# Performance work log

Measured on AMD Instinct MI355X. Metric: run time of the kernel, lower is better.

## Reference

```python
import jax, jax.numpy as jnp
import numpy as np

D = 256; NH = 8; NL = 3; NP = 4; DFF = 1024; NENC = 3; NDEC = 3; BS = 8
SHAPES = ((60, 60), (30, 30), (15, 15))
NQ = 3600

def _linear(x, W, b):
    return x @ W.T + b

def _ln(x, g, b, eps=1e-5):
    m = x.mean(-1, keepdims=True)
    v = ((x - m) ** 2).mean(-1, keepdims=True)
    return (x - m) / jnp.sqrt(v + eps) * g + b

def _pos_embed(h, w):
    # PositionEmbeddingSine(num_pos_feats=D//2, normalize=True)
    npf = D // 2
    scale = 2.0 * np.pi; eps = 1e-6
    ye = jnp.arange(1, h + 1, dtype=jnp.float32) / (h + eps) * scale
    xe = jnp.arange(1, w + 1, dtype=jnp.float32) / (w + eps) * scale
    dim_t = 10000.0 ** (2.0 * (jnp.arange(npf) // 2).astype(jnp.float32) / npf)
    def inter(p):  # interleave sin/cos like torch stack(...,4).flatten(3)
        return jnp.stack([jnp.sin(p[:, 0::2]), jnp.cos(p[:, 1::2])], -1).reshape(p.shape[0], npf)
    px = inter(xe[:, None] / dim_t)  # [w, npf]
    py = inter(ye[:, None] / dim_t)  # [h, npf]
    pos = jnp.concatenate([jnp.broadcast_to(py[:, None, :], (h, w, npf)),
                           jnp.broadcast_to(px[None, :, :], (h, w, npf))], -1)
    return pos.reshape(h * w, D)

def _grid(H, W):
    ry = (jnp.arange(H, dtype=jnp.float32) + 0.5) / H
    rx = (jnp.arange(W, dtype=jnp.float32) + 0.5) / W
    gy, gx = jnp.meshgrid(ry, rx, indexing='ij')
    return jnp.stack([gx.reshape(-1), gy.reshape(-1)], -1)

def _ref_enc():
    ref = jnp.concatenate([_grid(H, W) for (H, W) in SHAPES], 0)
    return jnp.broadcast_to(ref[None, :, None, :], (1, ref.shape[0], NL, 2))

def _ref_dec():
    ref = _grid(60, 60)  # hardcoded in DecoderLayer.get_reference_points
    return jnp.broadcast_to(ref[None, :, None, :], (1, NQ, NL, 2))

def _bilinear(v, x, y, H, W):
    # v: [N,h,HW,dh], x/y: [N,Lq,h,P] in pixel coords (grid_sample align_corners=False, zero padding)
    N, h, _, dh = v.shape
    Lq, P = x.shape[1], x.shape[3]
    x0 = jnp.floor(x); y0 = jnp.floor(y)
    wx1 = x - x0; wy1 = y - y0
    acc = jnp.zeros((N, h, Lq * P, dh), v.dtype)
    for dx, dy in ((0, 0), (1, 0), (0, 1), (1, 1)):
        xi = x0 + dx; yi = y0 + dy
        wgt = (wx1 if dx else 1.0 - wx1) * (wy1 if dy else 1.0 - wy1)
        valid = (xi >= 0) & (xi < W) & (yi >= 0) & (yi < H)
        idx = (jnp.clip(yi, 0, H - 1) * W + jnp.clip(xi, 0, W - 1)).astype(jnp.int32)
        idx = idx.transpose(0, 2, 1, 3).reshape(N, h, Lq * P)
        g = jnp.take_along_axis(v, idx[..., None], axis=2)
        wv = jnp.where(valid, wgt, 0.0).transpose(0, 2, 1, 3).reshape(N, h, Lq * P)
        acc = acc + g * wv[..., None]
    return acc.reshape(N, h, Lq, P, dh).transpose(0, 2, 1, 3, 4)  # [N,Lq,h,P,dh]

def _msda(query, ref, src, offW, offb, awW, awb, vpW, vpb, opW, opb):
    # Deformable-DETR MSDeformAttn
    N, Lq, d = query.shape
    h = NH; dh = d // h; P = NP
    value = _linear(src, vpW, vpb).reshape(N, -1, h, dh)
    off = _linear(query, offW, offb).reshape(N, Lq, h, NL, P, 2)
    aw = jax.nn.softmax(_linear(query, awW, awb).reshape(N, Lq, h, NL * P), -1).reshape(N, Lq, h, NL, P)
    norm = jnp.array([[W_, H_] for (H_, W_) in SHAPES], dtype=jnp.float32)
    loc = ref[:, :, None, :, None, :] + off / norm[None, None, None, :, None, :]
    out = jnp.zeros((N, Lq, h, dh), query.dtype)
    start = 0
    for l, (H_, W_) in enumerate(SHAPES):
        v = value[:, start:start + H_ * W_].transpose(0, 2, 1, 3)  # [N,h,HW,dh]
        start += H_ * W_
        lx = loc[:, :, :, l, :, 0] * W_ - 0.5
        ly = loc[:, :, :, l, :, 1] * H_ - 0.5
        s = _bilinear(v, lx, ly, H_, W_)
        out = out + (s * aw[:, :, :, l, :, None]).sum(3)
    return _linear(out.reshape(N, Lq, d), opW, opb)

def _mha(q, k, v, Wi, bi, Wo, bo):
    # torch nn.MultiheadAttention, inputs (L, N, E)
    L, N, E = q.shape
    h = NH; hd = E // h
    qp = _linear(q, Wi[:E], bi[:E]).reshape(L, N, h, hd)
    kp = _linear(k, Wi[E:2 * E], bi[E:2 * E]).reshape(L, N, h, hd)
    vp = _linear(v, Wi[2 * E:], bi[2 * E:]).reshape(L, N, h, hd)
    sc = jnp.einsum('lnhd,snhd->nhls', qp, kp) / np.float32(np.sqrt(hd))
    a = jax.nn.softmax(sc, -1)
    o = jnp.einsum('nhls,snhd->lnhd', a, vp).reshape(L, N, E)
    return _linear(o, Wo, bo)

def _forward(feat0, feat1, feat2, context, query_embed, level_embed, enc_off_W, enc_off_b, enc_aw_W, enc_aw_b, enc_vp_W, enc_vp_b, enc_op_W, enc_op_b, enc_fc1_W, enc_fc1_b, enc_fc2_W, enc_fc2_b, enc_ln1_g, enc_ln1_b, enc_ln2_g, enc_ln2_b, dec_off_W, dec_off_b, dec_aw_W, dec_aw_b, dec_vp_W, dec_vp_b, dec_op_W, dec_op_b, dec_fc1_W, dec_fc1_b, dec_fc2_W, dec_fc2_b, dec_ln1_g, dec_ln1_b, dec_ln2_g, dec_ln2_b, dec_sa_in_W, dec_sa_in_b, dec_sa_out_W, dec_sa_out_b, dec_ln3_g, dec_ln3_b):
    srcs, poss = [], []
    for l, (f, (H, W)) in enumerate(zip((feat0, feat1, feat2), SHAPES)):
        srcs.append(f.reshape(BS, D, H * W).transpose(0, 2, 1))
        pe = _pos_embed(H, W) + level_embed[l]
        poss.append(jnp.broadcast_to(pe[None], (BS, H * W, D)))
    src = jnp.concatenate(srcs, 1)   # [BS, S, D]
    pos = jnp.concatenate(poss, 1)
    ref_e = _ref_enc()
    out = src
    for i in range(NENC):
        a = _msda(out + pos, ref_e, out, enc_off_W[i], enc_off_b[i], enc_aw_W[i], enc_aw_b[i], enc_vp_W[i], enc_vp_b[i], enc_op_W[i], enc_op_b[i])
        out = _ln(out + a, enc_ln1_g[i], enc_ln1_b[i])
        f2 = _linear(jax.nn.relu(_linear(out, enc_fc1_W[i], enc_fc1_b[i])), enc_fc2_W[i], enc_fc2_b[i])
        out = _ln(out + f2, enc_ln2_g[i], enc_ln2_b[i])
    memory = out
    tgt = context + query_embed[:, None, :]  # [NQ, BS, D]
    ref_d = _ref_dec()
    for i in range(NDEC):
        # faithful to original: q.transpose(0,1) feeds MHA with (L=BS, N=NQ)
        q = tgt.transpose(1, 0, 2)
        t2 = _mha(q, q, q, dec_sa_in_W[i], dec_sa_in_b[i], dec_sa_out_W[i], dec_sa_out_b[i]).transpose(1, 0, 2)
        tgt = _ln(tgt + t2, dec_ln2_g[i], dec_ln2_b[i])
        tq = tgt.transpose(1, 0, 2)  # [BS, NQ, D]
        t2 = _msda(tq, ref_d, memory, dec_off_W[i], dec_off_b[i], dec_aw_W[i], dec_aw_b[i], dec_vp_W[i], dec_vp_b[i], dec_op_W[i], dec_op_b[i])
        tq = _ln(tq + t2, dec_ln1_g[i], dec_ln1_b[i])
        f2 = _linear(jax.nn.relu(_linear(tq, dec_fc1_W[i], dec_fc1_b[i])), dec_fc2_W[i], dec_fc2_b[i])
        tq = _ln(tq + f2, dec_ln3_g[i], dec_ln3_b[i])
        tgt = tq.transpose(1, 0, 2)
    return tgt  # [NQ, BS, D]

def setup_inputs() -> dict:
    key = jax.random.key(0)
    ks = iter(jax.random.split(key, 64))
    def rn(shape, s=1.0):
        return jax.random.normal(next(ks), shape, jnp.float32) * s
    inp = {}
    inp['feat0'] = rn((BS, D, 60, 60))
    inp['feat1'] = rn((BS, D, 30, 30))
    inp['feat2'] = rn((BS, D, 15, 15))
    inp['context'] = rn((NQ, BS, D))
    inp['query_embed'] = rn((NQ, D))
    inp['level_embed'] = rn((NL, D), 0.02)
    HLP2 = NH * NL * NP * 2; HLP = NH * NL * NP
    for pre, n in (('enc', NENC), ('dec', NDEC)):
        inp[pre + '_off_W'] = rn((n, HLP2, D), 0.02)
        inp[pre + '_off_b'] = rn((n, HLP2), 0.02)
        inp[pre + '_aw_W'] = rn((n, HLP, D), 0.02)
        inp[pre + '_aw_b'] = jnp.zeros((n, HLP), jnp.float32)
        inp[pre + '_vp_W'] = rn((n, D, D), 0.02)
        inp[pre + '_vp_b'] = jnp.zeros((n, D), jnp.float32)
        inp[pre + '_op_W'] = rn((n, D, D), 0.02)
        inp[pre + '_op_b'] = jnp.zeros((n, D), jnp.float32)
        inp[pre + '_fc1_W'] = rn((n, DFF, D), 0.02)
        inp[pre + '_fc1_b'] = jnp.zeros((n, DFF), jnp.float32)
        inp[pre + '_fc2_W'] = rn((n, D, DFF), 0.02)
        inp[pre + '_fc2_b'] = jnp.zeros((n, D), jnp.float32)
        inp[pre + '_ln1_g'] = jnp.ones((n, D), jnp.float32)
        inp[pre + '_ln1_b'] = jnp.zeros((n, D), jnp.float32)
        inp[pre + '_ln2_g'] = jnp.ones((n, D), jnp.float32)
        inp[pre + '_ln2_b'] = jnp.zeros((n, D), jnp.float32)
    inp['dec_sa_in_W'] = rn((NDEC, 3 * D, D), 0.02)
    inp['dec_sa_in_b'] = jnp.zeros((NDEC, 3 * D), jnp.float32)
    inp['dec_sa_out_W'] = rn((NDEC, D, D), 0.02)
    inp['dec_sa_out_b'] = jnp.zeros((NDEC, D), jnp.float32)
    inp['dec_ln3_g'] = jnp.ones((NDEC, D), jnp.float32)
    inp['dec_ln3_b'] = jnp.zeros((NDEC, D), jnp.float32)
    return inp

def reference(feat0, feat1, feat2, context, query_embed, level_embed, enc_off_W, enc_off_b, enc_aw_W, enc_aw_b, enc_vp_W, enc_vp_b, enc_op_W, enc_op_b, enc_fc1_W, enc_fc1_b, enc_fc2_W, enc_fc2_b, enc_ln1_g, enc_ln1_b, enc_ln2_g, enc_ln2_b, dec_off_W, dec_off_b, dec_aw_W, dec_aw_b, dec_vp_W, dec_vp_b, dec_op_W, dec_op_b, dec_fc1_W, dec_fc1_b, dec_fc2_W, dec_fc2_b, dec_ln1_g, dec_ln1_b, dec_ln2_g, dec_ln2_b, dec_sa_in_W, dec_sa_in_b, dec_sa_out_W, dec_sa_out_b, dec_ln3_g, dec_ln3_b):
    return _forward(feat0, feat1, feat2, context, query_embed, level_embed, enc_off_W, enc_off_b, enc_aw_W, enc_aw_b, enc_vp_W, enc_vp_b, enc_op_W, enc_op_b, enc_fc1_W, enc_fc1_b, enc_fc2_W, enc_fc2_b, enc_ln1_g, enc_ln1_b, enc_ln2_g, enc_ln2_b, dec_off_W, dec_off_b, dec_aw_W, dec_aw_b, dec_vp_W, dec_vp_b, dec_op_W, dec_op_b, dec_fc1_W, dec_fc1_b, dec_fc2_W, dec_fc2_b, dec_ln1_g, dec_ln1_b, dec_ln2_g, dec_ln2_b, dec_sa_in_W, dec_sa_in_b, dec_sa_out_W, dec_sa_out_b, dec_ln3_g, dec_ln3_b)
```

## Files before the change

kernel.cpp:

```cpp
#include <hip/hip_runtime.h>
#include <cmath>

#define D_MODEL 256
#define NHEADS 8
#define BSZ 8
#define S_TOT 4725
#define NQRY 3600

typedef unsigned short ushortT;
using bf16x8  = __attribute__((ext_vector_type(8))) __bf16;
using floatx4 = __attribute__((ext_vector_type(4))) float;

__device__ __forceinline__ ushortT f2bf(float f)
{
    union { float f; unsigned u; } v; v.f = f;
    unsigned r = v.u + 0x7FFFu + ((v.u >> 16) & 1u);
    return (ushortT)(r >> 16);
}
__device__ __forceinline__ float bf2f(ushortT u)
{
    union { unsigned u; float f; } v; v.u = ((unsigned)u) << 16;
    return v.f;
}
__device__ __forceinline__ float bits2f(unsigned u)
{
    union { unsigned u; float f; } v; v.u = u;
    return v.f;
}

#define GLD16(gp, lp) __builtin_amdgcn_global_load_lds( \
    (const __attribute__((address_space(1))) void*)(gp), \
    (__attribute__((address_space(3))) void*)(lp), 16, 0, 0)

template<int RELU, int OUTBF>
__global__ __launch_bounds__(256) void gemm_bf16_kernel(
    const ushortT* __restrict__ A, const ushortT* __restrict__ W,
    const float* __restrict__ bias, void* __restrict__ Cout,
    int M, int N, int K)
{
    __shared__ ushortT SM[128 * 32 * 2];
    ushortT* As = SM;
    ushortT* Bs = SM + 128 * 32;
    const int tid  = threadIdx.x;
    const int lane = tid & 63;
    const int wid  = tid >> 6;
    const int bm = blockIdx.x * 128;
    const int bn = blockIdx.y * 128;
    const int wm = (wid & 1) * 64;
    const int wn = (wid >> 1) * 64;
    const int col16 = lane & 15;
    const int quad  = lane >> 4;
    const int srow = lane >> 2;
    const int cperm = (lane & 3) ^ ((lane >> 3) & 3);
    const int rxor = (col16 >> 1) & 3;

    floatx4 acc[4][4];
#pragma unroll
    for (int i = 0; i < 4; i++)
#pragma unroll
        for (int j = 0; j < 4; j++) acc[i][j] = (floatx4){0.f, 0.f, 0.f, 0.f};

    const int rbase = wid * 32;
    for (int k0 = 0; k0 < K; k0 += 32) {
        if (k0) __syncthreads();
#pragma unroll
        for (int j = 0; j < 2; j++) {
            int row = rbase + j * 16 + srow;
            int gm = bm + row; if (gm >= M) gm = M - 1;
            GLD16(A + (size_t)gm * K + k0 + cperm * 8, &As[(rbase + j * 16) * 32]);
            int gn = bn + row; if (gn >= N) gn = N - 1;
            GLD16(W + (size_t)gn * K + k0 + cperm * 8, &Bs[(rbase + j * 16) * 32]);
        }
        __syncthreads();
        bf16x8 av[4], bv[4];
#pragma unroll
        for (int i = 0; i < 4; i++) {
            av[i] = *(const bf16x8*)&As[(wm + i * 16 + col16) * 32 + (quad ^ rxor) * 8];
            bv[i] = *(const bf16x8*)&Bs[(wn + i * 16 + col16) * 32 + (quad ^ rxor) * 8];
        }
#pragma unroll
        for (int mi = 0; mi < 4; mi++)
#pragma unroll
            for (int ni = 0; ni < 4; ni++)
                acc[mi][ni] = __builtin_amdgcn_mfma_f32_16x16x32_bf16(
                    av[mi], bv[ni], acc[mi][ni], 0, 0, 0);
    }

    if (OUTBF) {
        __syncthreads();
        ushortT* cs = SM + wid * (16 * 72);
        const int row_l = lane >> 2;
        const int colg  = (lane & 3) * 16;
#pragma unroll
        for (int mi = 0; mi < 4; mi++) {
#pragma unroll
            for (int ni = 0; ni < 4; ni++) {
                int gn = bn + wn + ni * 16 + col16;
                float bs = bias[gn < N ? gn : N - 1];
#pragma unroll
                for (int r = 0; r < 4; r++) {
                    float v = acc[mi][ni][r] + bs;
                    if (RELU) v = fmaxf(v, 0.f);
                    cs[(quad * 4 + r) * 72 + ni * 16 + col16] = f2bf(v);
                }
            }
            int gm = bm + wm + mi * 16 + row_l;
            int gn0 = bn + wn + colg;
            if (gm < M) {
                ushortT* dst = (ushortT*)Cout + (size_t)gm * N + gn0;
                if (gn0 + 8 <= N)  *(uint4*)dst       = *(uint4*)&cs[row_l * 72 + colg];
                if (gn0 + 16 <= N) *(uint4*)(dst + 8) = *(uint4*)&cs[row_l * 72 + colg + 8];
            }
        }
    } else {
#pragma unroll
        for (int ni = 0; ni < 4; ni++) {
            int gn = bn + wn + ni * 16 + col16;
            if (gn >= N) continue;
            float bs = bias[gn];
#pragma unroll
            for (int mi = 0; mi < 4; mi++) {
#pragma unroll
                for (int r = 0; r < 4; r++) {
                    int gm = bm + wm + mi * 16 + quad * 4 + r;
                    if (gm >= M) continue;
                    float v = acc[mi][ni][r] + bs;
                    if (RELU) v = fmaxf(v, 0.f);
                    ((float*)Cout)[(size_t)gm * N + gn] = v;
                }
            }
        }
    }
}

static inline void gemm_bf16(const ushortT* A, const ushortT* W, const float* bias,
                             void* C, int M, int N, int K, int relu, int outbf,
                             hipStream_t s)
{
    dim3 g((M + 127) / 128, (N + 127) / 128);
    if (relu) {
        if (outbf) hipLaunchKernelGGL((gemm_bf16_kernel<1,1>), g, dim3(256), 0, s, A, W, bias, C, M, N, K);
        else       hipLaunchKernelGGL((gemm_bf16_kernel<1,0>), g, dim3(256), 0, s, A, W, bias, C, M, N, K);
    } else {
        if (outbf) hipLaunchKernelGGL((gemm_bf16_kernel<0,1>), g, dim3(256), 0, s, A, W, bias, C, M, N, K);
        else       hipLaunchKernelGGL((gemm_bf16_kernel<0,0>), g, dim3(256), 0, s, A, W, bias, C, M, N, K);
    }
}

__global__ void f2bf_kernel(const float* __restrict__ src, ushortT* __restrict__ dst, int n)
{
    int t = blockIdx.x * blockDim.x + threadIdx.x;
    if (t < n) dst[t] = f2bf(src[t]);
}

__global__ void conv_offaw_kernel(const float* __restrict__ offW, const float* __restrict__ awW,
                                  ushortT* __restrict__ dst)
{
    int t = blockIdx.x * blockDim.x + threadIdx.x;
    if (t >= 3 * 288 * 256) return;
    int c = t & 255;
    int r = (t >> 8) % 288;
    int i = t / (288 * 256);
    float v = (r < 192) ? offW[((size_t)i * 192 + r) * 256 + c]
                        : awW[((size_t)i * 96 + (r - 192)) * 256 + c];
    dst[t] = f2bf(v);
}

__global__ void conv_offaw_bias_kernel(const float* __restrict__ offb, const float* __restrict__ awb,
                                       float* __restrict__ dst)
{
    int t = blockIdx.x * blockDim.x + threadIdx.x;
    if (t >= 3 * 288) return;
    int r = t % 288;
    int i = t / 288;
    dst[t] = (r < 192) ? offb[i * 192 + r] : awb[i * 96 + (r - 192)];
}

__device__ __forceinline__ void level_of(int s, int& l, int& H, int& W, int& hw)
{
    if (s < 3600)      { l = 0; H = 60; W = 60; hw = s; }
    else if (s < 4500) { l = 1; H = 30; W = 30; hw = s - 3600; }
    else               { l = 2; H = 15; W = 15; hw = s - 4500; }
}

__global__ __launch_bounds__(256) void transpose_feat_kernel(
    const float* __restrict__ f, ushortT* __restrict__ Xh, int HW, int s0)
{
    __shared__ float tile[32][33];
    const int b  = blockIdx.z;
    const int hw0 = blockIdx.x * 32;
    const int d0  = blockIdx.y * 32;
    const int tx = threadIdx.x & 31;
    const int ty = threadIdx.x >> 5;
    const float* fb = f + ((size_t)b * 256 + d0) * HW + hw0;
#pragma unroll
    for (int r = ty; r < 32; r += 8) {
        if (hw0 + tx < HW) tile[r][tx] = fb[(size_t)r * HW + tx];
    }
    __syncthreads();
    ushortT* xb = Xh + ((size_t)b * S_TOT + s0 + hw0) * 256 + d0;
#pragma unroll
    for (int r = ty; r < 32; r += 8) {
        if (hw0 + r < HW) xb[(size_t)r * 256 + tx] = f2bf(tile[tx][r]);
    }
}

__global__ void build_pos_kernel(const float* __restrict__ level_embed, float* __restrict__ pos)
{
    int t = blockIdx.x * blockDim.x + threadIdx.x;
    if (t >= S_TOT * D_MODEL) return;
    int d = t & 255;
    int s = t >> 8;
    int l, H, W, hw; level_of(s, l, H, W, hw);
    int y = hw / W, x = hw % W;
    int dd = (d < 128) ? d : d - 128;
    float v = (d < 128)
        ? ((float)(y + 1)) / ((float)H + 1e-6f) * 6.28318530717958647692f
        : ((float)(x + 1)) / ((float)W + 1e-6f) * 6.28318530717958647692f;
    float tpow = powf(10000.f, (float)(2 * (dd >> 1)) * (1.f / 128.f));
    float arg = v / tpow;
    float val = (dd & 1) ? cosf(arg) : sinf(arg);
    pos[t] = val + level_embed[l * D_MODEL + d];
}

__global__ void build_ref_kernel(float* __restrict__ refE, float* __restrict__ refD)
{
    int t = blockIdx.x * blockDim.x + threadIdx.x;
    if (t < S_TOT) {
        int l, H, W, hw; level_of(t, l, H, W, hw);
        int y = hw / W, x = hw % W;
        refE[2 * t]     = ((float)x + 0.5f) / (float)W;
        refE[2 * t + 1] = ((float)y + 0.5f) / (float)H;
    } else if (t < S_TOT + NQRY) {
        int q = t - S_TOT;
        int y = q / 60, x = q % 60;
        refD[2 * q]     = ((float)x + 0.5f) / 60.f;
        refD[2 * q + 1] = ((float)y + 0.5f) / 60.f;
    }
}

__global__ void build_tgt_kernel(const float* __restrict__ context, const float* __restrict__ qe,
                                 ushortT* __restrict__ TGTh)
{
    int t = blockIdx.x * blockDim.x + threadIdx.x;
    if (t >= NQRY * BSZ * 64) return;
    int gi = t & 63;
    int row = t >> 6;
    int nq = row >> 3;
    int d0 = gi * 4;
    const float4 c4 = *(const float4*)(context + (size_t)row * 256 + d0);
    const float4 q4 = *(const float4*)(qe + (size_t)nq * 256 + d0);
    ushortT pk[4] = { f2bf(c4.x + q4.x), f2bf(c4.y + q4.y), f2bf(c4.z + q4.z), f2bf(c4.w + q4.w) };
    *(uint2*)(TGTh + (size_t)row * 256 + d0) = *(uint2*)pk;
}

__global__ void add_pos_kernel(const ushortT* __restrict__ Xh, const float* __restrict__ pos,
                               ushortT* __restrict__ Qh)
{
    int t = blockIdx.x * blockDim.x + threadIdx.x;
    if (t >= BSZ * S_TOT * 64) return;
    int gi = t & 63;
    int row = t >> 6;
    int s = row % S_TOT;
    int d0 = gi * 4;
    ushortT x4[4];
    *(uint2*)x4 = *(const uint2*)(Xh + (size_t)row * 256 + d0);
    const float4 p4 = *(const float4*)(pos + (size_t)s * 256 + d0);
    ushortT pk[4] = { f2bf(bf2f(x4[0]) + p4.x), f2bf(bf2f(x4[1]) + p4.y),
                      f2bf(bf2f(x4[2]) + p4.z), f2bf(bf2f(x4[3]) + p4.w) };
    *(uint2*)(Qh + (size_t)row * 256 + d0) = *(uint2*)pk;
}

#define MROWS 8
__global__ __launch_bounds__(256) void msda_kernel(
    const ushortT* __restrict__ value, const float* __restrict__ oa,
    const float* __restrict__ ref, ushortT* __restrict__ out,
    int mode, int total_rows)
{
    __shared__ float sOff[MROWS][192];
    __shared__ float sW[MROWS][96];
    const int br0 = blockIdx.x * MROWS;

    for (int idx = threadIdx.x; idx < MROWS * 288; idx += 256) {
        int r = idx / 288, c = idx - r * 288;
        int lm = br0 + r;
        float v = (lm < total_rows) ? oa[(size_t)lm * 288 + c] : 0.f;
        if (c < 192) sOff[r][c] = v;
        else         sW[r][c - 192] = v;
    }
    __syncthreads();
    if (threadIdx.x < 64) {
        int r = threadIdx.x >> 3, h = threadIdx.x & 7;
        float* p = &sW[r][h * 12];
        float mx = p[0];
#pragma unroll
        for (int i = 1; i < 12; i++) mx = fmaxf(mx, p[i]);
        float ssum = 0.f;
        float e[12];
#pragma unroll
        for (int i = 0; i < 12; i++) { e[i] = expf(p[i] - mx); ssum += e[i]; }
        float inv = 1.f / ssum;
#pragma unroll
        for (int i = 0; i < 12; i++) p[i] = e[i] * inv;
    }
    __syncthreads();

    const int r  = threadIdx.x >> 5;
    const int h  = (threadIdx.x >> 2) & 7;
    const int cg = threadIdx.x & 3;
    const int lm = br0 + r;
    if (lm >= total_rows) return;
    int b, q;
    if (mode == 0) { b = lm / S_TOT; q = lm - b * S_TOT; }
    else           { q = lm >> 3;    b = lm & 7; }
    const float rx = ref[2 * q], ry = ref[2 * q + 1];
    const float* offp = &sOff[r][h * 24];
    const float* wp   = &sW[r][h * 12];

    float acc[8] = {};
    const int HWs[3][3] = {{60, 60, 0}, {30, 30, 3600}, {15, 15, 4500}};
#pragma unroll
    for (int l = 0; l < 3; l++) {
        const int H = HWs[l][0], W = HWs[l][1], s0 = HWs[l][2];
        const ushortT* vbase = value + ((size_t)b * S_TOT + s0) * 256 + h * 32 + cg * 8;
        const float fW = (float)W, fH = (float)H;
#pragma unroll 1
        for (int p = 0; p < 4; p++) {
            float ox = offp[(l * 4 + p) * 2];
            float oy = offp[(l * 4 + p) * 2 + 1];
            float w  = wp[l * 4 + p];
            float lx = rx * fW + ox - 0.5f;
            float ly = ry * fH + oy - 0.5f;
            float x0f = floorf(lx), y0f = floorf(ly);
            int x0 = (int)x0f, y0 = (int)y0f;
            float wx1 = lx - x0f, wy1 = ly - y0f;
            float mx0 = ((unsigned)x0       < (unsigned)W) ? (1.f - wx1) : 0.f;
            float mx1 = ((unsigned)(x0 + 1) < (unsigned)W) ? wx1         : 0.f;
            float my0 = ((unsigned)y0       < (unsigned)H) ? (1.f - wy1) : 0.f;
            float my1 = ((unsigned)(y0 + 1) < (unsigned)H) ? wy1         : 0.f;
            int xc0 = min(max(x0, 0), W - 1);
            int xc1 = min(max(x0 + 1, 0), W - 1);
            int yc0 = min(max(y0, 0), H - 1);
            int yc1 = min(max(y0 + 1, 0), H - 1);
            const uint4 v00 = *(const uint4*)(vbase + (size_t)(yc0 * W + xc0) * 256);
            const uint4 v01 = *(const uint4*)(vbase + (size_t)(yc0 * W + xc1) * 256);
            const uint4 v10 = *(const uint4*)(vbase + (size_t)(yc1 * W + xc0) * 256);
            const uint4 v11 = *(const uint4*)(vbase + (size_t)(yc1 * W + xc1) * 256);
            float w00 = w * my0 * mx0, w01 = w * my0 * mx1;
            float w10 = w * my1 * mx0, w11 = w * my1 * mx1;
#define ACC4(i, lo00, lo01, lo10, lo11) \
            acc[i] = fmaf(w00, bits2f(lo00), acc[i]); \
            acc[i] = fmaf(w01, bits2f(lo01), acc[i]); \
            acc[i] = fmaf(w10, bits2f(lo10), acc[i]); \
            acc[i] = fmaf(w11, bits2f(lo11), acc[i]);
            ACC4(0, v00.x << 16, v01.x << 16, v10.x << 16, v11.x << 16)
            ACC4(1, v00.x & 0xFFFF0000u, v01.x & 0xFFFF0000u, v10.x & 0xFFFF0000u, v11.x & 0xFFFF0000u)
            ACC4(2, v00.y << 16, v01.y << 16, v10.y << 16, v11.y << 16)
            ACC4(3, v00.y & 0xFFFF0000u, v01.y & 0xFFFF0000u, v10.y & 0xFFFF0000u, v11.y & 0xFFFF0000u)
            ACC4(4, v00.z << 16, v01.z << 16, v10.z << 16, v11.z << 16)
            ACC4(5, v00.z & 0xFFFF0000u, v01.z & 0xFFFF0000u, v10.z & 0xFFFF0000u, v11.z & 0xFFFF0000u)
            ACC4(6, v00.w << 16, v01.w << 16, v10.w << 16, v11.w << 16)
            ACC4(7, v00.w & 0xFFFF0000u, v01.w & 0xFFFF0000u, v10.w & 0xFFFF0000u, v11.w & 0xFFFF0000u)
#undef ACC4
        }
    }
    ushortT pk[8];
#pragma unroll
    for (int i = 0; i < 8; i++) pk[i] = f2bf(acc[i]);
    *(uint4*)(out + (size_t)lm * 256 + h * 32 + cg * 8) = *(uint4*)pk;
}

__global__ void ln_res_kernel(const ushortT* __restrict__ x, const ushortT* __restrict__ a,
                              const float* __restrict__ g, const float* __restrict__ b,
                              ushortT* __restrict__ outh, float* __restrict__ outf, int M)
{
    int wave = threadIdx.x >> 6;
    int lane = threadIdx.x & 63;
    int row = blockIdx.x * 4 + wave;
    if (row >= M) return;
    const int d0 = lane * 4;
    ushortT x4[4], a4[4];
    *(uint2*)x4 = *(const uint2*)(x + (size_t)row * 256 + d0);
    *(uint2*)a4 = *(const uint2*)(a + (size_t)row * 256 + d0);
    float v[4];
    float s = 0.f;
#pragma unroll
    for (int i = 0; i < 4; i++) { v[i] = bf2f(x4[i]) + bf2f(a4[i]); s += v[i]; }
#pragma unroll
    for (int o = 32; o > 0; o >>= 1) s += __shfl_down(s, o);
    s = __shfl(s, 0);
    float mean = s * (1.f / 256.f);
    float vs = 0.f;
#pragma unroll
    for (int i = 0; i < 4; i++) { float d = v[i] - mean; vs += d * d; }
#pragma unroll
    for (int o = 32; o > 0; o >>= 1) vs += __shfl_down(vs, o);
    vs = __shfl(vs, 0);
    float inv = rsqrtf(vs * (1.f / 256.f) + 1e-5f);
    const float4 g4 = *(const float4*)(g + d0);
    const float4 b4 = *(const float4*)(b + d0);
    float o0 = (v[0] - mean) * inv * g4.x + b4.x;
    float o1 = (v[1] - mean) * inv * g4.y + b4.y;
    float o2 = (v[2] - mean) * inv * g4.z + b4.z;
    float o3 = (v[3] - mean) * inv * g4.w + b4.w;
    ushortT pk[4] = { f2bf(o0), f2bf(o1), f2bf(o2), f2bf(o3) };
    *(uint2*)(outh + (size_t)row * 256 + d0) = *(uint2*)pk;
    if (outf) {
        float4 of = { o0, o1, o2, o3 };
        *(float4*)(outf + (size_t)row * 256 + d0) = of;
    }
}

__global__ void mha_kernel(const ushortT* __restrict__ qkv, ushortT* __restrict__ o, int nCnt)
{
    int t = blockIdx.x * blockDim.x + threadIdx.x;
    if (t >= nCnt * 64) return;
    int l = t & 7;
    int h = (t >> 3) & 7;
    int n = t >> 6;
    const ushortT* qp = qkv + (size_t)(n * 8 + l) * 768 + h * 32;
    float q[32];
#pragma unroll
    for (int d = 0; d < 32; d++) q[d] = bf2f(qp[d]);
    float sc[8];
#pragma unroll
    for (int s = 0; s < 8; s++) {
        const ushortT* kp = qkv + (size_t)(n * 8 + s) * 768 + 256 + h * 32;
        float acc = 0.f;
#pragma unroll
        for (int d = 0; d < 32; d++) acc = fmaf(q[d], bf2f(kp[d]), acc);
        sc[s] = acc * 0.17677669529663688f;
    }
    float mx = sc[0];
#pragma unroll
    for (int s = 1; s < 8; s++) mx = fmaxf(mx, sc[s]);
    float sum = 0.f;
#pragma unroll
    for (int s = 0; s < 8; s++) { sc[s] = expf(sc[s] - mx); sum += sc[s]; }
    float inv = 1.f / sum;
    float outv[32] = {};
#pragma unroll
    for (int s = 0; s < 8; s++) {
        const ushortT* vp = qkv + (size_t)(n * 8 + s) * 768 + 512 + h * 32;
        float a = sc[s] * inv;
#pragma unroll
        for (int d = 0; d < 32; d++) outv[d] = fmaf(a, bf2f(vp[d]), outv[d]);
    }
    ushortT* op = o + (size_t)(n * 8 + l) * 256 + h * 32;
#pragma unroll
    for (int d = 0; d < 32; d++) op[d] = f2bf(outv[d]);
}

extern "C" void kernel_launch(void* const* d_in, const int* in_sizes, int n_in,
                              void* d_out, int out_size, void* d_ws, size_t ws_size,
                              hipStream_t stream)
{
    const float* feat0       = (const float*)d_in[0];
    const float* feat1       = (const float*)d_in[1];
    const float* feat2       = (const float*)d_in[2];
    const float* context     = (const float*)d_in[3];
    const float* query_embed = (const float*)d_in[4];
    const float* level_embed = (const float*)d_in[5];
    const float* enc_off_W = (const float*)d_in[6];
    const float* enc_off_b = (const float*)d_in[7];
    const float* enc_aw_W  = (const float*)d_in[8];
    const float* enc_aw_b  = (const float*)d_in[9];
    const float* enc_vp_W  = (const float*)d_in[10];
    const float* enc_vp_b  = (const float*)d_in[11];
    const float* enc_op_W  = (const float*)d_in[12];
    const float* enc_op_b  = (const float*)d_in[13];
    const float* enc_fc1_W = (const float*)d_in[14];
    const float* enc_fc1_b = (const float*)d_in[15];
    const float* enc_fc2_W = (const float*)d_in[16];
    const float* enc_fc2_b = (const float*)d_in[17];
    const float* enc_ln1_g = (const float*)d_in[18];
    const float* enc_ln1_b = (const float*)d_in[19];
    const float* enc_ln2_g = (const float*)d_in[20];
    const float* enc_ln2_b = (const float*)d_in[21];
    const float* dec_off_W = (const float*)d_in[22];
    const float* dec_off_b = (const float*)d_in[23];
    const float* dec_aw_W  = (const float*)d_in[24];
    const float* dec_aw_b  = (const float*)d_in[25];
    const float* dec_vp_W  = (const float*)d_in[26];
    const float* dec_vp_b  = (const float*)d_in[27];
    const float* dec_op_W  = (const float*)d_in[28];
    const float* dec_op_b  = (const float*)d_in[29];
    const float* dec_fc1_W = (const float*)d_in[30];
    const float* dec_fc1_b = (const float*)d_in[31];
    const float* dec_fc2_W = (const float*)d_in[32];
    const float* dec_fc2_b = (const float*)d_in[33];
    const float* dec_ln1_g = (const float*)d_in[34];
    const float* dec_ln1_b = (const float*)d_in[35];
    const float* dec_ln2_g = (const float*)d_in[36];
    const float* dec_ln2_b = (const float*)d_in[37];
    const float* sa_in_W   = (const float*)d_in[38];
    const float* sa_in_b   = (const float*)d_in[39];
    const float* sa_out_W  = (const float*)d_in[40];
    const float* sa_out_b  = (const float*)d_in[41];
    const float* dec_ln3_g = (const float*)d_in[42];
    const float* dec_ln3_b = (const float*)d_in[43];

    const int ME = BSZ * S_TOT;
    const int MD = BSZ * NQRY;
    const int EW = ME * D_MODEL;
    const int DW = MD * D_MODEL;

    char* base = (char*)d_ws;
    size_t off = 0;
    auto alloc = [&](size_t bytes) -> char* {
        char* p = base + off;
        off += (bytes + 255) & ~(size_t)255;
        return p;
    };
    ushortT* Xh    = (ushortT*)alloc((size_t)EW * 2);
    ushortT* Vh    = (ushortT*)alloc((size_t)EW * 2);
    ushortT* TGTh  = (ushortT*)alloc((size_t)DW * 2);
    float*   POSb  = (float*)alloc((size_t)S_TOT * 256 * 4);
    float*   REFEb = (float*)alloc((size_t)S_TOT * 2 * 4);
    float*   REFDb = (float*)alloc((size_t)NQRY * 2 * 4);
    ushortT* Wbf   = (ushortT*)alloc((size_t)5160960 * 2);
    float*   OBIAS = (float*)alloc((size_t)2 * 3 * 288 * 4);
    ushortT* Yh    = (ushortT*)alloc((size_t)ME * 256 * 2);
    char*    R     = alloc((size_t)82252800);
    if (ws_size < off) return;

    ushortT* Qh   = (ushortT*)R;
    float*   OAf  = (float*)(R + 19353600);
    ushortT* OUTh = (ushortT*)(R + 62899200);
    ushortT* HIDh = (ushortT*)R;
    ushortT* QKVh = (ushortT*)R;
    ushortT* SOh  = (ushortT*)(R + 44236800);

    size_t wo = 0;
    auto walloc = [&](size_t elems) -> ushortT* { ushortT* p = Wbf + wo; wo += elems; return p; };
    ushortT* h_enc_offaw = walloc(3 * 288 * 256);
    ushortT* h_enc_vp    = walloc(3 * 65536);
    ushortT* h_enc_op    = walloc(3 * 65536);
    ushortT* h_enc_fc1   = walloc(3 * 262144);
    ushortT* h_enc_fc2   = walloc(3 * 262144);
    ushortT* h_dec_offaw = walloc(3 * 288 * 256);
    ushortT* h_dec_vp    = walloc(3 * 65536);
    ushortT* h_dec_op    = walloc(3 * 65536);
    ushortT* h_dec_fc1   = walloc(3 * 262144);
    ushortT* h_dec_fc2   = walloc(3 * 262144);
    ushortT* h_sa_in     = walloc(3 * 196608);
    ushortT* h_sa_out    = walloc(3 * 65536);
    float* enc_oab = OBIAS;
    float* dec_oab = OBIAS + 3 * 288;

    auto conv = [&](const float* s, ushortT* d, int n) {
        hipLaunchKernelGGL(f2bf_kernel, dim3((n + 255) / 256), dim3(256), 0, stream, s, d, n);
    };
    hipLaunchKernelGGL(conv_offaw_kernel, dim3((3 * 288 * 256 + 255) / 256), dim3(256), 0, stream,
                       enc_off_W, enc_aw_W, h_enc_offaw);
    hipLaunchKernelGGL(conv_offaw_kernel, dim3((3 * 288 * 256 + 255) / 256), dim3(256), 0, stream,
                       dec_off_W, dec_aw_W, h_dec_offaw);
    hipLaunchKernelGGL(conv_offaw_bias_kernel, dim3(4), dim3(256), 0, stream,
                       enc_off_b, enc_aw_b, enc_oab);
    hipLaunchKernelGGL(conv_offaw_bias_kernel, dim3(4), dim3(256), 0, stream,
                       dec_off_b, dec_aw_b, dec_oab);
    conv(enc_vp_W,  h_enc_vp,  3 * 65536);
    conv(enc_op_W,  h_enc_op,  3 * 65536);
    conv(enc_fc1_W, h_enc_fc1, 3 * 262144);
    conv(enc_fc2_W, h_enc_fc2, 3 * 262144);
    conv(dec_vp_W,  h_dec_vp,  3 * 65536);
    conv(dec_op_W,  h_dec_op,  3 * 65536);
    conv(dec_fc1_W, h_dec_fc1, 3 * 262144);
    conv(dec_fc2_W, h_dec_fc2, 3 * 262144);
    conv(sa_in_W,   h_sa_in,   3 * 196608);
    conv(sa_out_W,  h_sa_out,  3 * 65536);

    hipLaunchKernelGGL(build_pos_kernel, dim3((S_TOT * 256 + 255) / 256), dim3(256), 0, stream,
                       level_embed, POSb);
    hipLaunchKernelGGL(build_ref_kernel, dim3((S_TOT + NQRY + 255) / 256), dim3(256), 0, stream,
                       REFEb, REFDb);
    hipLaunchKernelGGL(transpose_feat_kernel, dim3(113, 8, 8), dim3(256), 0, stream,
                       feat0, Xh, 3600, 0);
    hipLaunchKernelGGL(transpose_feat_kernel, dim3(29, 8, 8), dim3(256), 0, stream,
                       feat1, Xh, 900, 3600);
    hipLaunchKernelGGL(transpose_feat_kernel, dim3(8, 8, 8), dim3(256), 0, stream,
                       feat2, Xh, 225, 4500);
    hipLaunchKernelGGL(build_tgt_kernel, dim3((MD * 64 + 255) / 256), dim3(256), 0, stream,
                       context, query_embed, TGTh);

    for (int i = 0; i < 3; i++) {
        gemm_bf16(Xh, h_enc_vp + (size_t)i * 65536, enc_vp_b + i * 256, Vh, ME, 256, 256, 0, 1, stream);
        hipLaunchKernelGGL(add_pos_kernel, dim3((ME * 64 + 255) / 256), dim3(256), 0, stream,
                           Xh, POSb, Qh);
        gemm_bf16(Qh, h_enc_offaw + (size_t)i * 73728, enc_oab + i * 288, OAf, ME, 288, 256, 0, 0, stream);
        hipLaunchKernelGGL(msda_kernel, dim3((ME + MROWS - 1) / MROWS), dim3(256), 0, stream,
                           Vh, OAf, REFEb, OUTh, 0, ME);
        gemm_bf16(OUTh, h_enc_op + (size_t)i * 65536, enc_op_b + i * 256, Yh, ME, 256, 256, 0, 1, stream);
        hipLaunchKernelGGL(ln_res_kernel, dim3((ME + 3) / 4), dim3(256), 0, stream,
                           Xh, Yh, enc_ln1_g + i * 256, enc_ln1_b + i * 256, Xh, (float*)nullptr, ME);
        gemm_bf16(Xh, h_enc_fc1 + (size_t)i * 262144, enc_fc1_b + i * 1024, HIDh, ME, 1024, 256, 1, 1, stream);
        gemm_bf16(HIDh, h_enc_fc2 + (size_t)i * 262144, enc_fc2_b + i * 256, Yh, ME, 256, 1024, 0, 1, stream);
        hipLaunchKernelGGL(ln_res_kernel, dim3((ME + 3) / 4), dim3(256), 0, stream,
                           Xh, Yh, enc_ln2_g + i * 256, enc_ln2_b + i * 256, Xh, (float*)nullptr, ME);
    }

    for (int i = 0; i < 3; i++) {
        gemm_bf16(TGTh, h_sa_in + (size_t)i * 196608, sa_in_b + i * 768, QKVh, MD, 768, 256, 0, 1, stream);
        hipLaunchKernelGGL(mha_kernel, dim3((MD * 8 + 255) / 256), dim3(256), 0, stream,
                           QKVh, SOh, MD / 8);
        gemm_bf16(SOh, h_sa_out + (size_t)i * 65536, sa_out_b + i * 256, Yh, MD, 256, 256, 0, 1, stream);
        hipLaunchKernelGGL(ln_res_kernel, dim3((MD + 3) / 4), dim3(256), 0, stream,
                           TGTh, Yh, dec_ln2_g + i * 256, dec_ln2_b + i * 256, TGTh, (float*)nullptr, MD);
        gemm_bf16(Xh, h_dec_vp + (size_t)i * 65536, dec_vp_b + i * 256, Vh, ME, 256, 256, 0, 1, stream);
        gemm_bf16(TGTh, h_dec_offaw + (size_t)i * 73728, dec_oab + i * 288, OAf, MD, 288, 256, 0, 0, stream);
        hipLaunchKernelGGL(msda_kernel, dim3((MD + MROWS - 1) / MROWS), dim3(256), 0, stream,
                           Vh, OAf, REFDb, OUTh, 1, MD);
        gemm_bf16(OUTh, h_dec_op + (size_t)i * 65536, dec_op_b + i * 256, Yh, MD, 256, 256, 0, 1, stream);
        hipLaunchKernelGGL(ln_res_kernel, dim3((MD + 3) / 4), dim3(256), 0, stream,
                           TGTh, Yh, dec_ln1_g + i * 256, dec_ln1_b + i * 256, TGTh, (float*)nullptr, MD);
        gemm_bf16(TGTh, h_dec_fc1 + (size_t)i * 262144, dec_fc1_b + i * 1024, HIDh, MD, 1024, 256, 1, 1, stream);
        gemm_bf16(HIDh, h_dec_fc2 + (size_t)i * 262144, dec_fc2_b + i * 256, Yh, MD, 256, 1024, 0, 1, stream);
        float* outf = (i == 2) ? (float*)d_out : nullptr;
        hipLaunchKernelGGL(ln_res_kernel, dim3((MD + 3) / 4), dim3(256), 0, stream,
                           TGTh, Yh, dec_ln3_g + i * 256, dec_ln3_b + i * 256, TGTh, outf, MD);
    }
}
```

Baseline: 1.646 ms.

## Fuse residual add and LayerNorm into output-projection and FC2 GEMM epilogues

Adds a GEMM kernel whose tile covers 64 rows by the full 256 output columns. Its epilogue adds the bias and the residual, computes row mean and variance across the four waves through shared memory, and applies LayerNorm. It writes bf16 output in place, plus fp32 output on the final decoder layer. This replaces every GEMM followed by ln_res pair, removing the intermediate Yh buffer round trip and twelve kernel launches. In exchange the GEMM uses narrower 64-row tiles with no double buffering, and the variance is computed as E[x^2]-mean^2, which is slightly less numerically robust.

```diff
diff --git a/kernel.cpp b/kernel.cpp
--- a/kernel.cpp
+++ b/kernel.cpp
@@ -145,6 +145,160 @@
         if (outbf) hipLaunchKernelGGL((gemm_bf16_kernel<0,1>), g, dim3(256), 0, s, A, W, bias, C, M, N, K);
         else       hipLaunchKernelGGL((gemm_bf16_kernel<0,0>), g, dim3(256), 0, s, A, W, bias, C, M, N, K);
     }
+}
+
+template<int HAS_OUTF>
+__global__ __launch_bounds__(256) void gemm_ln_kernel(
+    const ushortT* __restrict__ A, const ushortT* __restrict__ W,
+    const float* __restrict__ bias, const ushortT* __restrict__ X,
+    const float* __restrict__ gg, const float* __restrict__ bb,
+    ushortT* __restrict__ outh, float* __restrict__ outf,
+    int M, int K)
+{
+    __shared__ ushortT SM[320 * 32];
+    __shared__ float rs[64][4];
+    __shared__ float rq[64][4];
+    __shared__ float meanv[64];
+    __shared__ float invv[64];
+    const int tid  = threadIdx.x;
+    const int lane = tid & 63;
+    const int wid  = tid >> 6;
+    const int bm = blockIdx.x * 64;
+    const int wn = wid * 64;
+    const int col16 = lane & 15;
+    const int quad  = lane >> 4;
+    const int srow = lane >> 2;
+    const int cperm = (lane & 3) ^ ((lane >> 3) & 3);
+    const int rxor = (col16 >> 1) & 3;
+
+    floatx4 acc[4][4];
+#pragma unroll
+    for (int i = 0; i < 4; i++)
+#pragma unroll
+        for (int j = 0; j < 4; j++) acc[i][j] = (floatx4){0.f, 0.f, 0.f, 0.f};
+
+    for (int k0 = 0; k0 < K; k0 += 32) {
+        if (k0) __syncthreads();
+#pragma unroll
+        for (int j = 0; j < 5; j++) {
+            int frbase = wid * 80 + j * 16;
+            int fr = frbase + srow;
+            const ushortT* gp;
+            if (fr < 64) {
+                int gm = bm + fr; if (gm >= M) gm = M - 1;
+                gp = A + (size_t)gm * K + k0 + cperm * 8;
+            } else {
+                gp = W + (size_t)(fr - 64) * K + k0 + cperm * 8;
+            }
+            GLD16(gp, &SM[frbase * 32]);
+        }
+        __syncthreads();
+        bf16x8 av[4], bv[4];
+#pragma unroll
+        for (int i = 0; i < 4; i++) {
+            av[i] = *(const bf16x8*)&SM[(i * 16 + col16) * 32 + (quad ^ rxor) * 8];
+            bv[i] = *(const bf16x8*)&SM[(64 + wn + i * 16 + col16) * 32 + (quad ^ rxor) * 8];
+        }
+#pragma unroll
+        for (int mi = 0; mi < 4; mi++)
+#pragma unroll
+            for (int ni = 0; ni < 4; ni++)
+                acc[mi][ni] = __builtin_amdgcn_mfma_f32_16x16x32_bf16(
+                    av[mi], bv[ni], acc[mi][ni], 0, 0, 0);
+    }
+
+    int   gncol[4];
+    float bias4[4], gv[4], bbv[4];
+#pragma unroll
+    for (int ni = 0; ni < 4; ni++) {
+        gncol[ni] = wn + ni * 16 + col16;
+        bias4[ni] = bias[gncol[ni]];
+        gv[ni]    = gg[gncol[ni]];
+        bbv[ni]   = bb[gncol[ni]];
+    }
+
+    float psum[4][4], psq[4][4];
+#pragma unroll
+    for (int mi = 0; mi < 4; mi++) {
+#pragma unroll
+        for (int r = 0; r < 4; r++) {
+            int rowl = mi * 16 + quad * 4 + r;
+            int gmc = bm + rowl; if (gmc >= M) gmc = M - 1;
+            const ushortT* xp = X + (size_t)gmc * 256;
+            float ps = 0.f, pq = 0.f;
+#pragma unroll
+            for (int ni = 0; ni < 4; ni++) {
+                float v = acc[mi][ni][r] + bias4[ni] + bf2f(xp[gncol[ni]]);
+                acc[mi][ni][r] = v;
+                ps += v; pq += v * v;
+            }
+            psum[mi][r] = ps; psq[mi][r] = pq;
+        }
+    }
+#pragma unroll
+    for (int mi = 0; mi < 4; mi++) {
+#pragma unroll
+        for (int r = 0; r < 4; r++) {
+            float ps = psum[mi][r], pq = psq[mi][r];
+#pragma unroll
+            for (int m = 1; m < 16; m <<= 1) {
+                ps += __shfl_xor(ps, m);
+                pq += __shfl_xor(pq, m);
+            }
+            if (col16 == 0) {
+                int rowl = mi * 16 + quad * 4 + r;
+                rs[rowl][wid] = ps;
+                rq[rowl][wid] = pq;
+            }
+        }
+    }
+    __syncthreads();
+    if (tid < 64) {
+        float s = rs[tid][0] + rs[tid][1] + rs[tid][2] + rs[tid][3];
+        float q = rq[tid][0] + rq[tid][1] + rq[tid][2] + rq[tid][3];
+        float mean = s * (1.f / 256.f);
+        float var = q * (1.f / 256.f) - mean * mean;
+        meanv[tid] = mean;
+        invv[tid] = rsqrtf(var + 1e-5f);
+    }
+    __syncthreads();
+
+    ushortT* cs = SM + wid * (16 * 72);
+    const int row_l = lane >> 2;
+    const int colg  = (lane & 3) * 16;
+#pragma unroll
+    for (int mi = 0; mi < 4; mi++) {
+#pragma unroll
+        for (int ni = 0; ni < 4; ni++) {
+#pragma unroll
+            for (int r = 0; r < 4; r++) {
+                int rowl = mi * 16 + quad * 4 + r;
+                float outv = (acc[mi][ni][r] - meanv[rowl]) * invv[rowl] * gv[ni] + bbv[ni];
+                cs[(quad * 4 + r) * 72 + ni * 16 + col16] = f2bf(outv);
+                if (HAS_OUTF) {
+                    int gm = bm + rowl;
+                    if (gm < M) outf[(size_t)gm * 256 + gncol[ni]] = outv;
+                }
+            }
+        }
+        int gm = bm + mi * 16 + row_l;
+        if (gm < M) {
+            ushortT* dst = outh + (size_t)gm * 256 + wn + colg;
+            *(uint4*)dst       = *(uint4*)&cs[row_l * 72 + colg];
+            *(uint4*)(dst + 8) = *(uint4*)&cs[row_l * 72 + colg + 8];
+        }
+    }
+}
+
+static inline void gemm_ln(const ushortT* A, const ushortT* W, const float* bias,
+                           const ushortT* X, const float* g, const float* b,
+                           ushortT* outh, float* outf, int M, int K, hipStream_t s)
+{
+    dim3 grid((M + 63) / 64);
+    if (outf) hipLaunchKernelGGL((gemm_ln_kernel<1>), grid, dim3(256), 0, s,
+                                 A, W, bias, X, g, b, outh, outf, M, K);
+    else      hipLaunchKernelGGL((gemm_ln_kernel<0>), grid, dim3(256), 0, s,
+                                 A, W, bias, X, g, b, outh, (float*)nullptr, M, K);
 }
 
 __global__ void f2bf_kernel(const float* __restrict__ src, ushortT* __restrict__ dst, int n)
@@ -368,47 +522,6 @@
 #pragma unroll
     for (int i = 0; i < 8; i++) pk[i] = f2bf(acc[i]);
     *(uint4*)(out + (size_t)lm * 256 + h * 32 + cg * 8) = *(uint4*)pk;
-}
-
-__global__ void ln_res_kernel(const ushortT* __restrict__ x, const ushortT* __restrict__ a,
-                              const float* __restrict__ g, const float* __restrict__ b,
-                              ushortT* __restrict__ outh, float* __restrict__ outf, int M)
-{
-    int wave = threadIdx.x >> 6;
-    int lane = threadIdx.x & 63;
-    int row = blockIdx.x * 4 + wave;
-    if (row >= M) return;
-    const int d0 = lane * 4;
-    ushortT x4[4], a4[4];
-    *(uint2*)x4 = *(const uint2*)(x + (size_t)row * 256 + d0);
-    *(uint2*)a4 = *(const uint2*)(a + (size_t)row * 256 + d0);
-    float v[4];
-    float s = 0.f;
-#pragma unroll
-    for (int i = 0; i < 4; i++) { v[i] = bf2f(x4[i]) + bf2f(a4[i]); s += v[i]; }
-#pragma unroll
-    for (int o = 32; o > 0; o >>= 1) s += __shfl_down(s, o);
-    s = __shfl(s, 0);
-    float mean = s * (1.f / 256.f);
-    float vs = 0.f;
-#pragma unroll
-    for (int i = 0; i < 4; i++) { float d = v[i] - mean; vs += d * d; }
-#pragma unroll
-    for (int o = 32; o > 0; o >>= 1) vs += __shfl_down(vs, o);
-    vs = __shfl(vs, 0);
-    float inv = rsqrtf(vs * (1.f / 256.f) + 1e-5f);
-    const float4 g4 = *(const float4*)(g + d0);
-    const float4 b4 = *(const float4*)(b + d0);
-    float o0 = (v[0] - mean) * inv * g4.x + b4.x;
-    float o1 = (v[1] - mean) * inv * g4.y + b4.y;
-    float o2 = (v[2] - mean) * inv * g4.z + b4.z;
-    float o3 = (v[3] - mean) * inv * g4.w + b4.w;
-    ushortT pk[4] = { f2bf(o0), f2bf(o1), f2bf(o2), f2bf(o3) };
-    *(uint2*)(outh + (size_t)row * 256 + d0) = *(uint2*)pk;
-    if (outf) {
-        float4 of = { o0, o1, o2, o3 };
-        *(float4*)(outf + (size_t)row * 256 + d0) = of;
-    }
 }
 
 __global__ void mha_kernel(const ushortT* __restrict__ qkv, ushortT* __restrict__ o, int nCnt)
@@ -520,7 +633,6 @@
     float*   REFDb = (float*)alloc((size_t)NQRY * 2 * 4);
     ushortT* Wbf   = (ushortT*)alloc((size_t)5160960 * 2);
     float*   OBIAS = (float*)alloc((size_t)2 * 3 * 288 * 4);
-    ushortT* Yh    = (ushortT*)alloc((size_t)ME * 256 * 2);
     char*    R     = alloc((size_t)82252800);
     if (ws_size < off) return;
 
@@ -590,33 +702,28 @@
         gemm_bf16(Qh, h_enc_offaw + (size_t)i * 73728, enc_oab + i * 288, OAf, ME, 288, 256, 0, 0, stream);
         hipLaunchKernelGGL(msda_kernel, dim3((ME + MROWS - 1) / MROWS), dim3(256), 0, stream,
                            Vh, OAf, REFEb, OUTh, 0, ME);
-        gemm_bf16(OUTh, h_enc_op + (size_t)i * 65536, enc_op_b + i * 256, Yh, ME, 256, 256, 0, 1, stream);
-        hipLaunchKernelGGL(ln_res_kernel, dim3((ME + 3) / 4), dim3(256), 0, stream,
-                           Xh, Yh, enc_ln1_g + i * 256, enc_ln1_b + i * 256, Xh, (float*)nullptr, ME);
+        gemm_ln(OUTh, h_enc_op + (size_t)i * 65536, enc_op_b + i * 256,
+                Xh, enc_ln1_g + i * 256, enc_ln1_b + i * 256, Xh, nullptr, ME, 256, stream);
         gemm_bf16(Xh, h_enc_fc1 + (size_t)i * 262144, enc_fc1_b + i * 1024, HIDh, ME, 1024, 256, 1, 1, stream);
-        gemm_bf16(HIDh, h_enc_fc2 + (size_t)i * 262144, enc_fc2_b + i * 256, Yh, ME, 256, 1024, 0, 1, stream);
-        hipLaunchKernelGGL(ln_res_kernel, dim3((ME + 3) / 4), dim3(256), 0, stream,
-                           Xh, Yh, enc_ln2_g + i * 256, enc_ln2_b + i * 256, Xh, (float*)nullptr, ME);
+        gemm_ln(HIDh, h_enc_fc2 + (size_t)i * 262144, enc_fc2_b + i * 256,
+                Xh, enc_ln2_g + i * 256, enc_ln2_b + i * 256, Xh, nullptr, ME, 1024, stream);
     }
 
     for (int i = 0; i < 3; i++) {
         gemm_bf16(TGTh, h_sa_in + (size_t)i * 196608, sa_in_b + i * 768, QKVh, MD, 768, 256, 0, 1, stream);
         hipLaunchKernelGGL(mha_kernel, dim3((MD * 8 + 255) / 256), dim3(256), 0, stream,
                            QKVh, SOh, MD / 8);
-        gemm_bf16(SOh, h_sa_out + (size_t)i * 65536, sa_out_b + i * 256, Yh, MD, 256, 256, 0, 1, stream);
-        hipLaunchKernelGGL(ln_res_kernel, dim3((MD + 3) / 4), dim3(256), 0, stream,
-                           TGTh, Yh, dec_ln2_g + i * 256, dec_ln2_b + i * 256, TGTh, (float*)nullptr, MD);
+        gemm_ln(SOh, h_sa_out + (size_t)i * 65536, sa_out_b + i * 256,
+                TGTh, dec_ln2_g + i * 256, dec_ln2_b + i * 256, TGTh, nullptr, MD, 256, stream);
         gemm_bf16(Xh, h_dec_vp + (size_t)i * 65536, dec_vp_b + i * 256, Vh, ME, 256, 256, 0, 1, stream);
         gemm_bf16(TGTh, h_dec_offaw + (size_t)i * 73728, dec_oab + i * 288, OAf, MD, 288, 256, 0, 0, stream);
         hipLaunchKernelGGL(msda_kernel, dim3((MD + MROWS - 1) / MROWS), dim3(256), 0, stream,
                            Vh, OAf, REFDb, OUTh, 1, MD);
-        gemm_bf16(OUTh, h_dec_op + (size_t)i * 65536, dec_op_b + i * 256, Yh, MD, 256, 256, 0, 1, stream);
-        hipLaunchKernelGGL(ln_res_kernel, dim3((MD + 3) / 4), dim3(256), 0, stream,
-                           TGTh, Yh, dec_ln1_g + i * 256, dec_ln1_b + i * 256, TGTh, (float*)nullptr, MD);
+        gemm_ln(OUTh, h_dec_op + (size_t)i * 65536, dec_op_b + i * 256,
+                TGTh, dec_ln1_g + i * 256, dec_ln1_b + i * 256, TGTh, nullptr, MD, 256, stream);
         gemm_bf16(TGTh, h_dec_fc1 + (size_t)i * 262144, dec_fc1_b + i * 1024, HIDh, MD, 1024, 256, 1, 1, stream);
-        gemm_bf16(HIDh, h_dec_fc2 + (size_t)i * 262144, dec_fc2_b + i * 256, Yh, MD, 256, 1024, 0, 1, stream);
-        float* outf = (i == 2) ? (float*)d_out : nullptr;
-        hipLaunchKernelGGL(ln_res_kernel, dim3((MD + 3) / 4), dim3(256), 0, stream,
-                           TGTh, Yh, dec_ln3_g + i * 256, dec_ln3_b + i * 256, TGTh, outf, MD);
-    }
-}
+        gemm_ln(HIDh, h_dec_fc2 + (size_t)i * 262144, dec_fc2_b + i * 256,
+                TGTh, dec_ln3_g + i * 256, dec_ln3_b + i * 256, TGTh,
+                (i == 2) ? (float*)d_out : nullptr, MD, 1024, stream);
+    }
+}
```

New measurement: 1.646 ms. Within noise of the previous version (+0.0%).
